# Optimization experiments

Hardware: AMD Instinct MI355X
Metric: run time of the kernel (lower is better)

Reference implementation:

```python
import jax, jax.numpy as jnp
import numpy as np

B, S, H = 8, 2048, 768
N_SPANS = 512
MAX_SPAN_LEN = 30
WIDTH_VOCAB = 64
N_BIO, N_TYPE, N_SENS = 3, 18, 4
SPAN_DIM = H * 3 + H // 2  # 2688


def setup_inputs() -> dict:
    key = jax.random.key(0)
    ks = jax.random.split(key, 12)
    hidden = jax.random.normal(ks[0], (B, S, H), dtype=jnp.float32)
    # candidate spans: start in [0, S-MAX_SPAN_LEN), width in [1, MAX_SPAN_LEN]
    starts = jax.random.randint(ks[1], (B, N_SPANS), 0, S - MAX_SPAN_LEN)
    widths = jax.random.randint(ks[2], (B, N_SPANS), 1, MAX_SPAN_LEN + 1)
    ends = starts + widths - 1
    candidate_spans = jnp.stack([starts, ends], axis=-1).astype(jnp.int32)  # [B,N,2]
    sc = 0.02
    return {
        "hidden": hidden,
        "candidate_spans": candidate_spans,
        "width_emb": jax.random.normal(ks[3], (WIDTH_VOCAB, H // 2), dtype=jnp.float32) * sc,
        "W_prop": jax.random.normal(ks[4], (H, N_BIO), dtype=jnp.float32) * sc,
        "b_prop": jnp.zeros((N_BIO,), jnp.float32),
        "W_t1": jax.random.normal(ks[5], (SPAN_DIM, H), dtype=jnp.float32) * sc,
        "b_t1": jnp.zeros((H,), jnp.float32),
        "W_t2": jax.random.normal(ks[6], (H, N_TYPE), dtype=jnp.float32) * sc,
        "b_t2": jnp.zeros((N_TYPE,), jnp.float32),
        "W_s1": jax.random.normal(ks[7], (SPAN_DIM + N_TYPE, H), dtype=jnp.float32) * sc,
        "b_s1": jnp.zeros((H,), jnp.float32),
        "W_s2": jax.random.normal(ks[8], (H, N_SENS), dtype=jnp.float32) * sc,
        "b_s2": jnp.zeros((N_SENS,), jnp.float32),
    }


def _span_reprs(hidden, candidate_spans, width_emb):
    # hidden: [B,S,H], candidate_spans: [B,N,2] (all spans valid, 0 <= s <= e < S)
    starts = candidate_spans[..., 0]  # [B,N]
    ends = candidate_spans[..., 1]    # [B,N]
    gather = jax.vmap(lambda h, i: h[i])  # per-batch row gather
    start_h = gather(hidden, starts)  # [B,N,H]
    end_h = gather(hidden, ends)      # [B,N,H]
    # ragged mean-pool via inclusive prefix sums: sum(h[s:e+1]) = P[e+1]-P[s]
    P = jnp.concatenate(
        [jnp.zeros((hidden.shape[0], 1, hidden.shape[2]), hidden.dtype),
         jnp.cumsum(hidden, axis=1)], axis=1)  # [B,S+1,H]
    widths = ends - starts + 1  # [B,N]
    pooled = (gather(P, ends + 1) - gather(P, starts)) / widths[..., None].astype(hidden.dtype)
    width_h = width_emb[jnp.clip(widths, None, WIDTH_VOCAB - 1)]  # [B,N,H//2]
    return jnp.concatenate([start_h, end_h, pooled, width_h], axis=-1)  # [B,N,SPAN_DIM]


def reference(hidden, candidate_spans, width_emb, W_prop, b_prop,
              W_t1, b_t1, W_t2, b_t2, W_s1, b_s1, W_s2, b_s2):
    # proposal head (dropout = identity in eval)
    proposal_logits = hidden @ W_prop + b_prop  # [B,S,3]
    rep = _span_reprs(hidden, candidate_spans, width_emb)  # [B,N,2688]
    t = jax.nn.gelu(rep @ W_t1 + b_t1, approximate=False)
    type_logits = t @ W_t2 + b_t2  # [B,N,18]
    type_probs = jax.nn.softmax(type_logits, axis=-1)
    s_in = jnp.concatenate([rep, type_probs], axis=-1)  # [B,N,2706]
    s = jax.nn.gelu(s_in @ W_s1 + b_s1, approximate=False)
    sensitivity_logits = s @ W_s2 + b_s2  # [B,N,4]
    return proposal_logits, type_logits, sensitivity_logits
```

## Files before the change

### kernel.cpp

```cpp
#include <hip/hip_runtime.h>
#include <hip/hip_bf16.h>
#include <math.h>

#define Bn 8
#define Sn 2048
#define Hn 768
#define NROW 4096
#define SPAN_DIM 2688
#define NBIG 1536
#define NTYPE 18
#define NSENS 4
#define WPAD 24

typedef __attribute__((ext_vector_type(8))) short short8;
typedef __attribute__((ext_vector_type(4))) float floatx4;

__device__ __forceinline__ unsigned short f2bf(float x) {
    __hip_bfloat16 h = __float2bfloat16(x);
    return *reinterpret_cast<unsigned short*>(&h);
}

__device__ __forceinline__ float bfu(unsigned short u) {
    union { float f; unsigned int i; } v;
    v.i = ((unsigned int)u) << 16;
    return v.f;
}

__device__ __forceinline__ void glds16(const void* g, void* l) {
    __builtin_amdgcn_global_load_lds(
        (const __attribute__((address_space(1))) unsigned int*)g,
        (__attribute__((address_space(3))) unsigned int*)l, 16, 0, 0);
}

__device__ __forceinline__ float gelu_exact(float v) {
    return 0.5f * v * (1.f + erff(v * 0.70710678118654752f));
}

__global__ __launch_bounds__(256) void proposal_kernel(
    const float* __restrict__ hidden, const float* __restrict__ Wp,
    const float* __restrict__ bp, float* __restrict__ out)
{
    int wave = threadIdx.x >> 6;
    int lane = threadIdx.x & 63;
    int row  = blockIdx.x * 4 + wave;
    const float4* h4 = (const float4*)(hidden + (size_t)row * Hn);
    float a0 = 0.f, a1 = 0.f, a2 = 0.f;
#pragma unroll
    for (int i = 0; i < 3; ++i) {
        int kc = i * 64 + lane;
        float4 h = h4[kc];
        const float* w = Wp + kc * 12;
        a0 += h.x * w[0] + h.y * w[3] + h.z * w[6] + h.w * w[9];
        a1 += h.x * w[1] + h.y * w[4] + h.z * w[7] + h.w * w[10];
        a2 += h.x * w[2] + h.y * w[5] + h.z * w[8] + h.w * w[11];
    }
#pragma unroll
    for (int off = 32; off; off >>= 1) {
        a0 += __shfl_xor(a0, off);
        a1 += __shfl_xor(a1, off);
        a2 += __shfl_xor(a2, off);
    }
    if (lane < 3) {
        float v = (lane == 0 ? a0 : (lane == 1 ? a1 : a2)) + bp[lane];
        out[row * 3 + lane] = v;
    }
}

__global__ __launch_bounds__(192) void span_rep_kernel(
    const float* __restrict__ hidden, const int* __restrict__ spans,
    const float* __restrict__ wemb, unsigned short* __restrict__ rep)
{
    int n = blockIdx.x;
    int b = n >> 9;
    int s = spans[n * 2 + 0];
    int e = spans[n * 2 + 1];
    int w = e - s + 1;
    const float4* hb4 = (const float4*)(hidden + (size_t)b * Sn * Hn);
    unsigned short* r = rep + (size_t)n * SPAN_DIM;
    float inv_w = 1.0f / (float)w;
    int tid = threadIdx.x;

    float4 sv = hb4[(size_t)s * 192 + tid];
    float4 ev = hb4[(size_t)e * 192 + tid];
    float4 p0 = make_float4(0.f, 0.f, 0.f, 0.f), p1 = p0, p2 = p0, p3 = p0;
    int rr = s;
    for (; rr + 3 <= e; rr += 4) {
        float4 h0 = hb4[(size_t)(rr + 0) * 192 + tid];
        float4 h1 = hb4[(size_t)(rr + 1) * 192 + tid];
        float4 h2 = hb4[(size_t)(rr + 2) * 192 + tid];
        float4 h3 = hb4[(size_t)(rr + 3) * 192 + tid];
        p0.x += h0.x; p0.y += h0.y; p0.z += h0.z; p0.w += h0.w;
        p1.x += h1.x; p1.y += h1.y; p1.z += h1.z; p1.w += h1.w;
        p2.x += h2.x; p2.y += h2.y; p2.z += h2.z; p2.w += h2.w;
        p3.x += h3.x; p3.y += h3.y; p3.z += h3.z; p3.w += h3.w;
    }
    for (; rr <= e; ++rr) {
        float4 h = hb4[(size_t)rr * 192 + tid];
        p0.x += h.x; p0.y += h.y; p0.z += h.z; p0.w += h.w;
    }
    float4 pv;
    pv.x = ((p0.x + p1.x) + (p2.x + p3.x)) * inv_w;
    pv.y = ((p0.y + p1.y) + (p2.y + p3.y)) * inv_w;
    pv.z = ((p0.z + p1.z) + (p2.z + p3.z)) * inv_w;
    pv.w = ((p0.w + p1.w) + (p2.w + p3.w)) * inv_w;

    *(ushort4*)&r[tid * 4] =
        make_ushort4(f2bf(sv.x), f2bf(sv.y), f2bf(sv.z), f2bf(sv.w));
    *(ushort4*)&r[Hn + tid * 4] =
        make_ushort4(f2bf(ev.x), f2bf(ev.y), f2bf(ev.z), f2bf(ev.w));
    *(ushort4*)&r[2 * Hn + tid * 4] =
        make_ushort4(f2bf(pv.x), f2bf(pv.y), f2bf(pv.z), f2bf(pv.w));
    if (tid < 96) {
        int wi = w > 63 ? 63 : w;
        float4 wv = ((const float4*)wemb)[wi * 96 + tid];
        *(ushort4*)&r[3 * Hn + tid * 4] =
            make_ushort4(f2bf(wv.x), f2bf(wv.y), f2bf(wv.z), f2bf(wv.w));
    }
}

__global__ __launch_bounds__(256) void prep_weights(
    const float* __restrict__ Wt1, const float* __restrict__ Ws1,
    unsigned short* __restrict__ WbigT,
    const float* __restrict__ Wt2, const float* __restrict__ Ws2,
    unsigned short* __restrict__ Wt2bf, unsigned short* __restrict__ Wtailbf,
    unsigned short* __restrict__ Ws2bf)
{
    int z = blockIdx.z;
    if (z == 2) {
        int gid = blockIdx.y * 84 + blockIdx.x;
        int idx = gid * 256 + threadIdx.x;
        const int N1 = Hn * WPAD;
        const int N2 = 2 * N1;
        const int N3 = N2 + Hn * NSENS;
        if (idx < N1) {
            int k = idx / WPAD, o = idx - k * WPAD;
            Wt2bf[idx] = (o < NTYPE) ? f2bf(Wt2[k * NTYPE + o]) : 0;
        } else if (idx < N2) {
            int j = idx - N1;
            int k = j / WPAD, o = j - k * WPAD;
            Wtailbf[j] = (o < NTYPE) ? f2bf(Ws1[(size_t)(SPAN_DIM + o) * Hn + k]) : 0;
        } else if (idx < N3) {
            int j = idx - N2;
            Ws2bf[j] = f2bf(Ws2[j]);
        }
        return;
    }
    const float* W = (z == 0) ? Wt1 : Ws1;
    unsigned short* Wt = WbigT + (size_t)z * Hn * SPAN_DIM;
    __shared__ float tile[32][33];
    int k0 = blockIdx.x * 32, n0 = blockIdx.y * 32;
    int tx = threadIdx.x & 31, ty = threadIdx.x >> 5;
#pragma unroll
    for (int i = 0; i < 32; i += 8)
        tile[ty + i][tx] = W[(size_t)(k0 + ty + i) * Hn + n0 + tx];
    __syncthreads();
#pragma unroll
    for (int i = 0; i < 32; i += 8)
        Wt[(size_t)(n0 + ty + i) * SPAN_DIM + k0 + tx] = f2bf(tile[tx][ty + i]);
}

__global__ __launch_bounds__(256, 3) void gemm_fused(
    const unsigned short* __restrict__ A,
    const unsigned short* __restrict__ Bt,
    const float* __restrict__ bt1, const float* __restrict__ bs1,
    float* __restrict__ obuf)
{
    const int BK = 64;
    __shared__ unsigned short As[128 * BK];
    __shared__ unsigned short Bs[64 * BK];

    int tid = threadIdx.x, wave = tid >> 6, lane = tid & 63;
    int m0 = blockIdx.x * 128, n0 = blockIdx.y * 64;
    int wr = (wave >> 1) * 64;
    int wc = (wave & 1) * 32;
    int fr = lane & 15;
    int fc = lane >> 4;

    const unsigned short* gA[4];
#pragma unroll
    for (int j = 0; j < 4; ++j) {
        int d = tid + j * 256;
        int r = d >> 3, c = (d & 7) ^ (r & 7);
        gA[j] = A + (size_t)(m0 + r) * SPAN_DIM + c * 8;
    }
    const unsigned short* gB[2];
#pragma unroll
    for (int j = 0; j < 2; ++j) {
        int d = tid + j * 256;
        int r = d >> 3, c = (d & 7) ^ (r & 7);
        gB[j] = Bt + (size_t)(n0 + r) * SPAN_DIM + c * 8;
    }
    unsigned short* ldsA[4];
    unsigned short* ldsB[2];
#pragma unroll
    for (int j = 0; j < 4; ++j) ldsA[j] = As + j * 2048 + wave * 512;
#pragma unroll
    for (int j = 0; j < 2; ++j) ldsB[j] = Bs + j * 2048 + wave * 512;

    floatx4 acc[4][2] = {};

    for (int k0 = 0; k0 < SPAN_DIM; k0 += BK) {
        glds16(gA[0] + k0, ldsA[0]);
        glds16(gA[1] + k0, ldsA[1]);
        glds16(gA[2] + k0, ldsA[2]);
        glds16(gA[3] + k0, ldsA[3]);
        glds16(gB[0] + k0, ldsB[0]);
        glds16(gB[1] + k0, ldsB[1]);
        __syncthreads();

#pragma unroll
        for (int half = 0; half < 2; ++half) {
            int cb = half * 4 + fc;
            short8 af[4], bf[2];
#pragma unroll
            for (int i = 0; i < 4; ++i) {
                int r = wr + i * 16 + fr;
                af[i] = *(const short8*)&As[((r << 3) | (cb ^ (r & 7))) * 8];
            }
#pragma unroll
            for (int i = 0; i < 2; ++i) {
                int r = wc + i * 16 + fr;
                bf[i] = *(const short8*)&Bs[((r << 3) | (cb ^ (r & 7))) * 8];
            }
#pragma unroll
            for (int mi = 0; mi < 4; ++mi)
#pragma unroll
                for (int ni = 0; ni < 2; ++ni)
                    acc[mi][ni] = __builtin_amdgcn_mfma_f32_16x16x32_bf16(
                        af[mi], bf[ni], acc[mi][ni], 0, 0, 0);
        }
        __syncthreads();
    }

    bool isT = (n0 < Hn);
    const float* bias = isT ? bt1 : (bs1 - Hn);
    int cr = (lane >> 4) * 4;
#pragma unroll
    for (int mi = 0; mi < 4; ++mi) {
#pragma unroll
        for (int ni = 0; ni < 2; ++ni) {
            int col = n0 + wc + ni * 16 + fr;
            float bv = bias[col];
#pragma unroll
            for (int r = 0; r < 4; ++r) {
                int row = m0 + wr + mi * 16 + cr + r;
                float v = acc[mi][ni][r] + bv;
                if (isT) v = gelu_exact(v);
                obuf[(size_t)row * NBIG + col] = v;
            }
        }
    }
}

__global__ __launch_bounds__(256) void heads_kernel(
    const float* __restrict__ obuf, const unsigned short* __restrict__ Wt2bf,
    const float* __restrict__ bt2, const unsigned short* __restrict__ Wtailbf,
    const unsigned short* __restrict__ Ws2bf, const float* __restrict__ bs2,
    float* __restrict__ out_type, float* __restrict__ out_sens)
{
    int wave = threadIdx.x >> 6, lane = threadIdx.x & 63;
    int row = blockIdx.x * 4 + wave;
    const float* tr = obuf + (size_t)row * NBIG;

    float t[12];
    {
        const float4* t4 = (const float4*)(tr + lane * 12);
        float4 a = t4[0], b = t4[1], c = t4[2];
        t[0] = a.x; t[1] = a.y; t[2]  = a.z; t[3]  = a.w;
        t[4] = b.x; t[5] = b.y; t[6]  = b.z; t[7]  = b.w;
        t[8] = c.x; t[9] = c.y; t[10] = c.z; t[11] = c.w;
    }
    float acc[NTYPE] = {};
    const unsigned short* wp = Wt2bf + (size_t)lane * 12 * WPAD;
#pragma unroll
    for (int j = 0; j < 12; ++j) {
        short8 w0 = *(const short8*)(wp + j * WPAD);
        short8 w1 = *(const short8*)(wp + j * WPAD + 8);
        ushort4 w2 = *(const ushort4*)(wp + j * WPAD + 16);
        float tv = t[j];
#pragma unroll
        for (int o = 0; o < 8; ++o) acc[o] += tv * bfu((unsigned short)w0[o]);
#pragma unroll
        for (int o = 0; o < 8; ++o) acc[8 + o] += tv * bfu((unsigned short)w1[o]);
        acc[16] += tv * bfu(w2.x);
        acc[17] += tv * bfu(w2.y);
    }
#pragma unroll
    for (int o = 0; o < NTYPE; ++o)
#pragma unroll
        for (int off = 32; off; off >>= 1) acc[o] += __shfl_xor(acc[o], off);

    float mx = -1e30f;
#pragma unroll
    for (int o = 0; o < NTYPE; ++o) { acc[o] += bt2[o]; mx = fmaxf(mx, acc[o]); }
    {
        float lv = 0.f;
#pragma unroll
        for (int o = 0; o < NTYPE; ++o) lv = (lane == o) ? acc[o] : lv;
        if (lane < NTYPE) out_type[row * NTYPE + lane] = lv;
    }
    float pr[NTYPE], sum = 0.f;
#pragma unroll
    for (int o = 0; o < NTYPE; ++o) { pr[o] = expf(acc[o] - mx); sum += pr[o]; }
    float inv = 1.f / sum;
#pragma unroll
    for (int o = 0; o < NTYPE; ++o) pr[o] *= inv;

    float s[12];
    {
        const float4* s4 = (const float4*)(tr + Hn + lane * 12);
        float4 a = s4[0], b = s4[1], c = s4[2];
        s[0] = a.x; s[1] = a.y; s[2]  = a.z; s[3]  = a.w;
        s[4] = b.x; s[5] = b.y; s[6]  = b.z; s[7]  = b.w;
        s[8] = c.x; s[9] = c.y; s[10] = c.z; s[11] = c.w;
    }
    float acc2[NSENS] = {};
    const unsigned short* wt = Wtailbf + (size_t)lane * 12 * WPAD;
    const unsigned short* w2p = Ws2bf + (size_t)lane * 12 * NSENS;
#pragma unroll
    for (int j = 0; j < 12; ++j) {
        short8 a0 = *(const short8*)(wt + j * WPAD);
        short8 a1 = *(const short8*)(wt + j * WPAD + 8);
        ushort4 a2 = *(const ushort4*)(wt + j * WPAD + 16);
        float tl = 0.f;
#pragma unroll
        for (int o = 0; o < 8; ++o) tl += pr[o] * bfu((unsigned short)a0[o]);
#pragma unroll
        for (int o = 0; o < 8; ++o) tl += pr[8 + o] * bfu((unsigned short)a1[o]);
        tl += pr[16] * bfu(a2.x) + pr[17] * bfu(a2.y);
        float v = gelu_exact(s[j] + tl);
        ushort4 wv = *(const ushort4*)(w2p + j * NSENS);
        acc2[0] += v * bfu(wv.x);
        acc2[1] += v * bfu(wv.y);
        acc2[2] += v * bfu(wv.z);
        acc2[3] += v * bfu(wv.w);
    }
#pragma unroll
    for (int o = 0; o < NSENS; ++o)
#pragma unroll
        for (int off = 32; off; off >>= 1) acc2[o] += __shfl_xor(acc2[o], off);
    {
        float lv = 0.f;
#pragma unroll
        for (int o = 0; o < NSENS; ++o) lv = (lane == o) ? (acc2[o] + bs2[o]) : lv;
        if (lane < NSENS) out_sens[row * NSENS + lane] = lv;
    }
}

extern "C" void kernel_launch(void* const* d_in, const int* in_sizes, int n_in,
                              void* d_out, int out_size, void* d_ws, size_t ws_size,
                              hipStream_t stream)
{
    const float* hidden = (const float*)d_in[0];
    const int*   spans  = (const int*)d_in[1];
    const float* wemb   = (const float*)d_in[2];
    const float* Wp     = (const float*)d_in[3];
    const float* bp     = (const float*)d_in[4];
    const float* Wt1    = (const float*)d_in[5];
    const float* bt1    = (const float*)d_in[6];
    const float* Wt2    = (const float*)d_in[7];
    const float* bt2    = (const float*)d_in[8];
    const float* Ws1    = (const float*)d_in[9];
    const float* bs1    = (const float*)d_in[10];
    const float* Ws2    = (const float*)d_in[11];
    const float* bs2    = (const float*)d_in[12];

    float* out      = (float*)d_out;
    float* out_prop = out;
    float* out_type = out + Bn * Sn * 3;
    float* out_sens = out_type + NROW * NTYPE;

    unsigned short* rep = (unsigned short*)d_ws;
    float* obuf = (float*)(rep + (size_t)NROW * SPAN_DIM);
    unsigned short* WbigT = (unsigned short*)(obuf + (size_t)NROW * NBIG);
    unsigned short* Wt2bf   = WbigT + (size_t)NBIG * SPAN_DIM;
    unsigned short* Wtailbf = Wt2bf + Hn * WPAD;
    unsigned short* Ws2bf   = Wtailbf + Hn * WPAD;

    prep_weights<<<dim3(SPAN_DIM / 32, Hn / 32, 3), 256, 0, stream>>>(
        Wt1, Ws1, WbigT, Wt2, Ws2, Wt2bf, Wtailbf, Ws2bf);

    proposal_kernel<<<Bn * Sn / 4, 256, 0, stream>>>(hidden, Wp, bp, out_prop);
    span_rep_kernel<<<NROW, 192, 0, stream>>>(hidden, spans, wemb, rep);

    dim3 gg(NROW / 128, NBIG / 64);
    gemm_fused<<<gg, 256, 0, stream>>>(rep, WbigT, bt1, bs1, obuf);

    heads_kernel<<<NROW / 4, 256, 0, stream>>>(
        obuf, Wt2bf, bt2, Wtailbf, Ws2bf, bs2, out_type, out_sens);
}
```

Measured before the change: 218.8 us.

## Merge pre-GEMM kernels, double-buffer GEMM LDS, remap blocks for XCD locality

Folds weight prep, the proposal head and span representation into one launch that dispatches on block index. This removes two kernel launches and lets independent work overlap. The GEMM now double-buffers its A/B LDS tiles, prefetching the next K slice while computing the current one, which drops one barrier per iteration. Blocks are also remapped so each XCD gets a contiguous group of M tiles, to improve L2 reuse. Double buffering doubles LDS use, to 48KB per block, which may lower occupancy under the launch-bounds hint of 3 blocks.

```diff
diff --git a/kernel.cpp b/kernel.cpp
--- a/kernel.cpp
+++ b/kernel.cpp
@@ -12,6 +12,12 @@
 #define NSENS 4
 #define WPAD 24
 
+#define NB_PROP 4096
+#define NB_SPAN 4096
+#define NB_T    2016
+#define NB_SM   156
+#define NB_TOTAL (NB_PROP + NB_SPAN + 2 * NB_T + NB_SM)
+
 typedef __attribute__((ext_vector_type(8))) short short8;
 typedef __attribute__((ext_vector_type(4))) float floatx4;
 
@@ -36,99 +42,116 @@
     return 0.5f * v * (1.f + erff(v * 0.70710678118654752f));
 }
 
-__global__ __launch_bounds__(256) void proposal_kernel(
-    const float* __restrict__ hidden, const float* __restrict__ Wp,
-    const float* __restrict__ bp, float* __restrict__ out)
-{
-    int wave = threadIdx.x >> 6;
-    int lane = threadIdx.x & 63;
-    int row  = blockIdx.x * 4 + wave;
-    const float4* h4 = (const float4*)(hidden + (size_t)row * Hn);
-    float a0 = 0.f, a1 = 0.f, a2 = 0.f;
-#pragma unroll
-    for (int i = 0; i < 3; ++i) {
-        int kc = i * 64 + lane;
-        float4 h = h4[kc];
-        const float* w = Wp + kc * 12;
-        a0 += h.x * w[0] + h.y * w[3] + h.z * w[6] + h.w * w[9];
-        a1 += h.x * w[1] + h.y * w[4] + h.z * w[7] + h.w * w[10];
-        a2 += h.x * w[2] + h.y * w[5] + h.z * w[8] + h.w * w[11];
-    }
-#pragma unroll
-    for (int off = 32; off; off >>= 1) {
-        a0 += __shfl_xor(a0, off);
-        a1 += __shfl_xor(a1, off);
-        a2 += __shfl_xor(a2, off);
-    }
-    if (lane < 3) {
-        float v = (lane == 0 ? a0 : (lane == 1 ? a1 : a2)) + bp[lane];
-        out[row * 3 + lane] = v;
-    }
-}
-
-__global__ __launch_bounds__(192) void span_rep_kernel(
+__global__ __launch_bounds__(256) void pre_kernel(
     const float* __restrict__ hidden, const int* __restrict__ spans,
-    const float* __restrict__ wemb, unsigned short* __restrict__ rep)
-{
-    int n = blockIdx.x;
-    int b = n >> 9;
-    int s = spans[n * 2 + 0];
-    int e = spans[n * 2 + 1];
-    int w = e - s + 1;
-    const float4* hb4 = (const float4*)(hidden + (size_t)b * Sn * Hn);
-    unsigned short* r = rep + (size_t)n * SPAN_DIM;
-    float inv_w = 1.0f / (float)w;
-    int tid = threadIdx.x;
-
-    float4 sv = hb4[(size_t)s * 192 + tid];
-    float4 ev = hb4[(size_t)e * 192 + tid];
-    float4 p0 = make_float4(0.f, 0.f, 0.f, 0.f), p1 = p0, p2 = p0, p3 = p0;
-    int rr = s;
-    for (; rr + 3 <= e; rr += 4) {
-        float4 h0 = hb4[(size_t)(rr + 0) * 192 + tid];
-        float4 h1 = hb4[(size_t)(rr + 1) * 192 + tid];
-        float4 h2 = hb4[(size_t)(rr + 2) * 192 + tid];
-        float4 h3 = hb4[(size_t)(rr + 3) * 192 + tid];
-        p0.x += h0.x; p0.y += h0.y; p0.z += h0.z; p0.w += h0.w;
-        p1.x += h1.x; p1.y += h1.y; p1.z += h1.z; p1.w += h1.w;
-        p2.x += h2.x; p2.y += h2.y; p2.z += h2.z; p2.w += h2.w;
-        p3.x += h3.x; p3.y += h3.y; p3.z += h3.z; p3.w += h3.w;
-    }
-    for (; rr <= e; ++rr) {
-        float4 h = hb4[(size_t)rr * 192 + tid];
-        p0.x += h.x; p0.y += h.y; p0.z += h.z; p0.w += h.w;
-    }
-    float4 pv;
-    pv.x = ((p0.x + p1.x) + (p2.x + p3.x)) * inv_w;
-    pv.y = ((p0.y + p1.y) + (p2.y + p3.y)) * inv_w;
-    pv.z = ((p0.z + p1.z) + (p2.z + p3.z)) * inv_w;
-    pv.w = ((p0.w + p1.w) + (p2.w + p3.w)) * inv_w;
-
-    *(ushort4*)&r[tid * 4] =
-        make_ushort4(f2bf(sv.x), f2bf(sv.y), f2bf(sv.z), f2bf(sv.w));
-    *(ushort4*)&r[Hn + tid * 4] =
-        make_ushort4(f2bf(ev.x), f2bf(ev.y), f2bf(ev.z), f2bf(ev.w));
-    *(ushort4*)&r[2 * Hn + tid * 4] =
-        make_ushort4(f2bf(pv.x), f2bf(pv.y), f2bf(pv.z), f2bf(pv.w));
-    if (tid < 96) {
-        int wi = w > 63 ? 63 : w;
-        float4 wv = ((const float4*)wemb)[wi * 96 + tid];
-        *(ushort4*)&r[3 * Hn + tid * 4] =
-            make_ushort4(f2bf(wv.x), f2bf(wv.y), f2bf(wv.z), f2bf(wv.w));
-    }
-}
-
-__global__ __launch_bounds__(256) void prep_weights(
+    const float* __restrict__ wemb,
+    const float* __restrict__ Wp, const float* __restrict__ bp,
     const float* __restrict__ Wt1, const float* __restrict__ Ws1,
+    const float* __restrict__ Wt2, const float* __restrict__ Ws2,
+    float* __restrict__ out_prop, unsigned short* __restrict__ rep,
     unsigned short* __restrict__ WbigT,
-    const float* __restrict__ Wt2, const float* __restrict__ Ws2,
     unsigned short* __restrict__ Wt2bf, unsigned short* __restrict__ Wtailbf,
     unsigned short* __restrict__ Ws2bf)
 {
-    int z = blockIdx.z;
-    if (z == 2) {
-        int gid = blockIdx.y * 84 + blockIdx.x;
-        int idx = gid * 256 + threadIdx.x;
+    __shared__ float tile[32][33];
+    int id = blockIdx.x;
+    int tid = threadIdx.x;
+
+    if (id < NB_PROP) {
+        int wave = tid >> 6, lane = tid & 63;
+        int row = id * 4 + wave;
+        const float4* h4 = (const float4*)(hidden + (size_t)row * Hn);
+        float a0 = 0.f, a1 = 0.f, a2 = 0.f;
+#pragma unroll
+        for (int i = 0; i < 3; ++i) {
+            int kc = i * 64 + lane;
+            float4 h = h4[kc];
+            const float* w = Wp + kc * 12;
+            a0 += h.x * w[0] + h.y * w[3] + h.z * w[6] + h.w * w[9];
+            a1 += h.x * w[1] + h.y * w[4] + h.z * w[7] + h.w * w[10];
+            a2 += h.x * w[2] + h.y * w[5] + h.z * w[8] + h.w * w[11];
+        }
+#pragma unroll
+        for (int off = 32; off; off >>= 1) {
+            a0 += __shfl_xor(a0, off);
+            a1 += __shfl_xor(a1, off);
+            a2 += __shfl_xor(a2, off);
+        }
+        if (lane < 3) {
+            float v = (lane == 0 ? a0 : (lane == 1 ? a1 : a2)) + bp[lane];
+            out_prop[row * 3 + lane] = v;
+        }
+        return;
+    }
+    id -= NB_PROP;
+    if (id < NB_SPAN) {
+        if (tid >= 192) return;
+        int n = id;
+        int b = n >> 9;
+        int s = spans[n * 2 + 0];
+        int e = spans[n * 2 + 1];
+        int w = e - s + 1;
+        const float4* hb4 = (const float4*)(hidden + (size_t)b * Sn * Hn);
+        unsigned short* r = rep + (size_t)n * SPAN_DIM;
+        float inv_w = 1.0f / (float)w;
+
+        float4 sv = hb4[(size_t)s * 192 + tid];
+        float4 ev = hb4[(size_t)e * 192 + tid];
+        float4 p0 = make_float4(0.f, 0.f, 0.f, 0.f), p1 = p0, p2 = p0, p3 = p0;
+        int rr = s;
+        for (; rr + 3 <= e; rr += 4) {
+            float4 h0 = hb4[(size_t)(rr + 0) * 192 + tid];
+            float4 h1 = hb4[(size_t)(rr + 1) * 192 + tid];
+            float4 h2 = hb4[(size_t)(rr + 2) * 192 + tid];
+            float4 h3 = hb4[(size_t)(rr + 3) * 192 + tid];
+            p0.x += h0.x; p0.y += h0.y; p0.z += h0.z; p0.w += h0.w;
+            p1.x += h1.x; p1.y += h1.y; p1.z += h1.z; p1.w += h1.w;
+            p2.x += h2.x; p2.y += h2.y; p2.z += h2.z; p2.w += h2.w;
+            p3.x += h3.x; p3.y += h3.y; p3.z += h3.z; p3.w += h3.w;
+        }
+        for (; rr <= e; ++rr) {
+            float4 h = hb4[(size_t)rr * 192 + tid];
+            p0.x += h.x; p0.y += h.y; p0.z += h.z; p0.w += h.w;
+        }
+        float4 pv;
+        pv.x = ((p0.x + p1.x) + (p2.x + p3.x)) * inv_w;
+        pv.y = ((p0.y + p1.y) + (p2.y + p3.y)) * inv_w;
+        pv.z = ((p0.z + p1.z) + (p2.z + p3.z)) * inv_w;
+        pv.w = ((p0.w + p1.w) + (p2.w + p3.w)) * inv_w;
+
+        *(ushort4*)&r[tid * 4] =
+            make_ushort4(f2bf(sv.x), f2bf(sv.y), f2bf(sv.z), f2bf(sv.w));
+        *(ushort4*)&r[Hn + tid * 4] =
+            make_ushort4(f2bf(ev.x), f2bf(ev.y), f2bf(ev.z), f2bf(ev.w));
+        *(ushort4*)&r[2 * Hn + tid * 4] =
+            make_ushort4(f2bf(pv.x), f2bf(pv.y), f2bf(pv.z), f2bf(pv.w));
+        if (tid < 96) {
+            int wi = w > 63 ? 63 : w;
+            float4 wv = ((const float4*)wemb)[wi * 96 + tid];
+            *(ushort4*)&r[3 * Hn + tid * 4] =
+                make_ushort4(f2bf(wv.x), f2bf(wv.y), f2bf(wv.z), f2bf(wv.w));
+        }
+        return;
+    }
+    id -= NB_SPAN;
+    if (id < 2 * NB_T) {
+        int z = id / NB_T, l = id - z * NB_T;
+        const float* W = (z == 0) ? Wt1 : Ws1;
+        unsigned short* Wt = WbigT + (size_t)z * Hn * SPAN_DIM;
+        int k0 = (l % 84) * 32, n0 = (l / 84) * 32;
+        int tx = tid & 31, ty = tid >> 5;
+#pragma unroll
+        for (int i = 0; i < 32; i += 8)
+            tile[ty + i][tx] = W[(size_t)(k0 + ty + i) * Hn + n0 + tx];
+        __syncthreads();
+#pragma unroll
+        for (int i = 0; i < 32; i += 8)
+            Wt[(size_t)(n0 + ty + i) * SPAN_DIM + k0 + tx] = f2bf(tile[tx][ty + i]);
+        return;
+    }
+    id -= 2 * NB_T;
+    {
+        int idx = id * 256 + tid;
         const int N1 = Hn * WPAD;
         const int N2 = 2 * N1;
         const int N3 = N2 + Hn * NSENS;
@@ -143,20 +166,7 @@
             int j = idx - N2;
             Ws2bf[j] = f2bf(Ws2[j]);
         }
-        return;
-    }
-    const float* W = (z == 0) ? Wt1 : Ws1;
-    unsigned short* Wt = WbigT + (size_t)z * Hn * SPAN_DIM;
-    __shared__ float tile[32][33];
-    int k0 = blockIdx.x * 32, n0 = blockIdx.y * 32;
-    int tx = threadIdx.x & 31, ty = threadIdx.x >> 5;
-#pragma unroll
-    for (int i = 0; i < 32; i += 8)
-        tile[ty + i][tx] = W[(size_t)(k0 + ty + i) * Hn + n0 + tx];
-    __syncthreads();
-#pragma unroll
-    for (int i = 0; i < 32; i += 8)
-        Wt[(size_t)(n0 + ty + i) * SPAN_DIM + k0 + tx] = f2bf(tile[tx][ty + i]);
+    }
 }
 
 __global__ __launch_bounds__(256, 3) void gemm_fused(
@@ -166,11 +176,16 @@
     float* __restrict__ obuf)
 {
     const int BK = 64;
-    __shared__ unsigned short As[128 * BK];
-    __shared__ unsigned short Bs[64 * BK];
+    __shared__ unsigned short As[2][128 * BK];
+    __shared__ unsigned short Bs[2][64 * BK];
 
     int tid = threadIdx.x, wave = tid >> 6, lane = tid & 63;
-    int m0 = blockIdx.x * 128, n0 = blockIdx.y * 64;
+    int bid = blockIdx.x;
+    int xcd = bid & 7, g = bid >> 3;
+    int bx = xcd * 4 + (g / 24);
+    int by = g % 24;
+    int m0 = bx * 128, n0 = by * 64;
+
     int wr = (wave >> 1) * 64;
     int wc = (wave & 1) * 32;
     int fr = lane & 15;
@@ -190,37 +205,48 @@
         int r = d >> 3, c = (d & 7) ^ (r & 7);
         gB[j] = Bt + (size_t)(n0 + r) * SPAN_DIM + c * 8;
     }
-    unsigned short* ldsA[4];
-    unsigned short* ldsB[2];
-#pragma unroll
-    for (int j = 0; j < 4; ++j) ldsA[j] = As + j * 2048 + wave * 512;
-#pragma unroll
-    for (int j = 0; j < 2; ++j) ldsB[j] = Bs + j * 2048 + wave * 512;
+    int offA[4], offB[2];
+#pragma unroll
+    for (int j = 0; j < 4; ++j) offA[j] = j * 2048 + wave * 512;
+#pragma unroll
+    for (int j = 0; j < 2; ++j) offB[j] = j * 2048 + wave * 512;
 
     floatx4 acc[4][2] = {};
 
-    for (int k0 = 0; k0 < SPAN_DIM; k0 += BK) {
-        glds16(gA[0] + k0, ldsA[0]);
-        glds16(gA[1] + k0, ldsA[1]);
-        glds16(gA[2] + k0, ldsA[2]);
-        glds16(gA[3] + k0, ldsA[3]);
-        glds16(gB[0] + k0, ldsB[0]);
-        glds16(gB[1] + k0, ldsB[1]);
+    glds16(gA[0], &As[0][offA[0]]);
+    glds16(gA[1], &As[0][offA[1]]);
+    glds16(gA[2], &As[0][offA[2]]);
+    glds16(gA[3], &As[0][offA[3]]);
+    glds16(gB[0], &Bs[0][offB[0]]);
+    glds16(gB[1], &Bs[0][offB[1]]);
+
+    const int NITER = SPAN_DIM / BK;
+    for (int i = 0; i < NITER; ++i) {
+        int cur = i & 1;
         __syncthreads();
-
+        if (i + 1 < NITER) {
+            int k1 = (i + 1) * BK;
+            int nxt = cur ^ 1;
+            glds16(gA[0] + k1, &As[nxt][offA[0]]);
+            glds16(gA[1] + k1, &As[nxt][offA[1]]);
+            glds16(gA[2] + k1, &As[nxt][offA[2]]);
+            glds16(gA[3] + k1, &As[nxt][offA[3]]);
+            glds16(gB[0] + k1, &Bs[nxt][offB[0]]);
+            glds16(gB[1] + k1, &Bs[nxt][offB[1]]);
+        }
 #pragma unroll
         for (int half = 0; half < 2; ++half) {
             int cb = half * 4 + fc;
             short8 af[4], bf[2];
 #pragma unroll
-            for (int i = 0; i < 4; ++i) {
-                int r = wr + i * 16 + fr;
-                af[i] = *(const short8*)&As[((r << 3) | (cb ^ (r & 7))) * 8];
+            for (int ii = 0; ii < 4; ++ii) {
+                int r = wr + ii * 16 + fr;
+                af[ii] = *(const short8*)&As[cur][((r << 3) | (cb ^ (r & 7))) * 8];
             }
 #pragma unroll
-            for (int i = 0; i < 2; ++i) {
-                int r = wc + i * 16 + fr;
-                bf[i] = *(const short8*)&Bs[((r << 3) | (cb ^ (r & 7))) * 8];
+            for (int ii = 0; ii < 2; ++ii) {
+                int r = wc + ii * 16 + fr;
+                bf[ii] = *(const short8*)&Bs[cur][((r << 3) | (cb ^ (r & 7))) * 8];
             }
 #pragma unroll
             for (int mi = 0; mi < 4; ++mi)
@@ -229,7 +255,6 @@
                     acc[mi][ni] = __builtin_amdgcn_mfma_f32_16x16x32_bf16(
                         af[mi], bf[ni], acc[mi][ni], 0, 0, 0);
         }
-        __syncthreads();
     }
 
     bool isT = (n0 < Hn);
@@ -377,14 +402,11 @@
     unsigned short* Wtailbf = Wt2bf + Hn * WPAD;
     unsigned short* Ws2bf   = Wtailbf + Hn * WPAD;
 
-    prep_weights<<<dim3(SPAN_DIM / 32, Hn / 32, 3), 256, 0, stream>>>(
-        Wt1, Ws1, WbigT, Wt2, Ws2, Wt2bf, Wtailbf, Ws2bf);
-
-    proposal_kernel<<<Bn * Sn / 4, 256, 0, stream>>>(hidden, Wp, bp, out_prop);
-    span_rep_kernel<<<NROW, 192, 0, stream>>>(hidden, spans, wemb, rep);
-
-    dim3 gg(NROW / 128, NBIG / 64);
-    gemm_fused<<<gg, 256, 0, stream>>>(rep, WbigT, bt1, bs1, obuf);
+    pre_kernel<<<NB_TOTAL, 256, 0, stream>>>(
+        hidden, spans, wemb, Wp, bp, Wt1, Ws1, Wt2, Ws2,
+        out_prop, rep, WbigT, Wt2bf, Wtailbf, Ws2bf);
+
+    gemm_fused<<<768, 256, 0, stream>>>(rep, WbigT, bt1, bs1, obuf);
 
     heads_kernel<<<NROW / 4, 256, 0, stream>>>(
         obuf, Wt2bf, bt2, Wtailbf, Ws2bf, bs2, out_type, out_sens);
```

Result: slower. 230.0 us (+5.1%).
